# Kernel optimization log

Hardware: AMD Instinct MI355X
Metric: run time of the kernel (lower is better)

## Reference

```python
import jax, jax.numpy as jnp
import numpy as np

E = 1024
H = 16
HD = E // H  # 64
R = 8
ALPHA = 32
SCALING = ALPHA / R  # LoRA scaling = 4.0


def _lora_linear(x, W, b, A, B):
    # x: [..., in], W: [out, in], A: [r, in], B: [out, r]
    base = jnp.einsum('...i,oi->...o', x, W) + b
    lora = jnp.einsum('...r,or->...o', jnp.einsum('...i,ri->...r', x, A), B) * SCALING
    return base + lora


def setup_inputs() -> dict:
    key = jax.random.key(0)
    ks = jax.random.split(key, 20)
    L, N = 2048, 2
    d = {}
    d['query'] = jax.random.normal(ks[0], (L, N, E), dtype=jnp.float32)
    d['key_padding_mask'] = jax.random.randint(ks[1], (N, L), 0, 2) > 0
    i = 2
    for p in ('q', 'k', 'v', 'o'):
        d['W' + p] = jax.random.normal(ks[i], (E, E), dtype=jnp.float32) * (E ** -0.5); i += 1
        d['b' + p] = jax.random.normal(ks[i], (E,), dtype=jnp.float32) * 0.01; i += 1
        d['A' + p] = jax.random.normal(ks[i], (R, E), dtype=jnp.float32) * (E ** -0.5); i += 1
        d['B' + p] = jax.random.normal(ks[i], (E, R), dtype=jnp.float32) * 0.01; i += 1
    return d


def reference(query, key_padding_mask, Wq, bq, Aq, Bq, Wk, bk, Ak, Bk,
              Wv, bv, Av, Bv, Wo, bo, Ao, Bo):
    L, N, _ = query.shape
    q = _lora_linear(query, Wq, bq, Aq, Bq)  # [L, N, E]
    k = _lora_linear(query, Wk, bk, Ak, Bk)
    v = _lora_linear(query, Wv, bv, Av, Bv)

    def split_heads(x):  # [L, N, E] -> [N, H, L, HD]
        return x.transpose(1, 0, 2).reshape(N, L, H, HD).transpose(0, 2, 1, 3)

    scale = HD ** -0.5
    qh = split_heads(q) * scale
    kh = split_heads(k)
    vh = split_heads(v)

    logits = jnp.einsum('nhqd,nhkd->nhqk', qh, kh)  # [N, H, L, L]
    dt = logits.dtype
    pad = key_padding_mask[:, None, None, :]  # [N, 1, 1, Lk]
    logits = jnp.where(pad, jnp.finfo(dt).min, logits)
    logits = logits - jnp.max(logits, axis=-1, keepdims=True)
    w = jax.nn.softmax(logits, axis=-1)
    # zero out padded keys then renormalize (faithful to the module)
    w = jnp.where(pad, jnp.zeros((), dt), w)
    denom = jnp.maximum(jnp.sum(w, axis=-1, keepdims=True), jnp.finfo(dt).tiny)
    w = w / denom

    out = jnp.einsum('nhqk,nhkd->nhqd', w, vh)  # [N, H, L, HD]
    out = out.transpose(0, 2, 1, 3).reshape(N, L, E).transpose(1, 0, 2)  # [L, N, E]
    attn_output = _lora_linear(out, Wo, bo, Ao, Bo)

    # average_attn_weights=True path: mean over heads, then permute(1,0,2)
    attn_weights_out = jnp.mean(w, axis=1).transpose(1, 0, 2)  # [Lq, N, Lk]
    return attn_output, attn_weights_out
```

## Files before the change

### kernel.cpp

```cpp
#include <hip/hip_runtime.h>
#include <stdint.h>


typedef __attribute__((ext_vector_type(8))) short short8;
typedef __attribute__((ext_vector_type(4))) float f32x4;

#define LORA_SCALING 4.0f
#define FTINY 1.1754943508222875e-38f

static __device__ __forceinline__ unsigned short f2bf(float f){
  unsigned u = __float_as_uint(f);
  u += 0x7fffu + ((u >> 16) & 1u);
  return (unsigned short)(u >> 16);
}
static __device__ __forceinline__ float bflo(unsigned u){ return __uint_as_float(u << 16); }
static __device__ __forceinline__ float bfhi(unsigned u){ return __uint_as_float(u & 0xffff0000u); }
static __device__ __forceinline__ unsigned pk2(float lo, float hi){
  return (unsigned)f2bf(lo) | ((unsigned)f2bf(hi) << 16);
}
static __device__ __forceinline__ unsigned cvtpk(float lo, float hi){
  unsigned r;
  asm("v_cvt_pk_bf16_f32 %0, %1, %2" : "=v"(r) : "v"(lo), "v"(hi));
  return r;
}
static __device__ __forceinline__ void gload16(const void* g, void* l){
  __builtin_amdgcn_global_load_lds(
      (const __attribute__((address_space(1))) unsigned int*)g,
      (__attribute__((address_space(3))) unsigned int*)l, 16, 0, 0);
}

union S8U { short8 v; uint2 u[2]; };

__global__ __launch_bounds__(256) void pack_bf16(const float* __restrict__ src,
                                                 unsigned short* __restrict__ dst)
{
  const size_t i = (size_t)blockIdx.x * 256 + threadIdx.x;
  const float4 f0 = ((const float4*)src)[i*2];
  const float4 f1 = ((const float4*)src)[i*2 + 1];
  ((uint4*)dst)[i] = make_uint4(pk2(f0.x,f0.y), pk2(f0.z,f0.w),
                                pk2(f1.x,f1.y), pk2(f1.z,f1.w));
}

__global__ __launch_bounds__(256) void xa_kernel(const unsigned short* __restrict__ X,
                                                 const float* __restrict__ A,
                                                 float* __restrict__ xa)
{
  __shared__ float red[4][8];
  const int t = blockIdx.x, tid = threadIdx.x;
  const int lane = tid & 63, wid = tid >> 6;

  const uint2 xr = *(const uint2*)(X + (size_t)t*1024 + tid*4);
  const float x0 = bflo(xr.x), x1 = bfhi(xr.x), x2 = bflo(xr.y), x3 = bfhi(xr.y);

  float acc[8];
#pragma unroll
  for (int r = 0; r < 8; ++r) {
    const float4 ar = *(const float4*)(A + (size_t)r*1024 + tid*4);
    acc[r] = x0*ar.x + x1*ar.y + x2*ar.z + x3*ar.w;
  }
#pragma unroll
  for (int r = 0; r < 8; ++r) {
    float v = acc[r];
#pragma unroll
    for (int off = 32; off > 0; off >>= 1) v += __shfl_xor(v, off, 64);
    if (lane == 0) red[wid][r] = v;
  }
  __syncthreads();
  if (tid < 8) xa[(size_t)t*8 + tid] = red[0][tid] + red[1][tid] + red[2][tid] + red[3][tid];
}

__global__ __launch_bounds__(256) void gemm_bf16(
    const unsigned short* __restrict__ Abf,
    const unsigned short* __restrict__ W0bf, const unsigned short* __restrict__ W1bf,
    const unsigned short* __restrict__ W2bf,
    const float* __restrict__ B0, const float* __restrict__ B1, const float* __restrict__ B2,
    const float* __restrict__ xa0, const float* __restrict__ xa1, const float* __restrict__ xa2,
    const float* __restrict__ L0, const float* __restrict__ L1, const float* __restrict__ L2,
    void* __restrict__ C0, void* __restrict__ C1, void* __restrict__ C2,
    int fp32out, float scale0)
{
  const int z = blockIdx.z;
  const unsigned short* W = (z==0)?W0bf:((z==1)?W1bf:W2bf);
  const float* Bb = (z==0)?B0:((z==1)?B1:B2);
  const float* xa = (z==0)?xa0:((z==1)?xa1:xa2);
  const float* Lb = (z==0)?L0:((z==1)?L1:L2);
  void*        C  = (z==0)?C0:((z==1)?C1:C2);
  const bool vtw = (z == 2);
  const float sc = (z == 0) ? scale0 : 1.0f;

  __shared__ alignas(16) unsigned short As[128*32];
  __shared__ alignas(16) unsigned short Bs[128*32];

  const int tid = threadIdx.x;
  const int lane = tid & 63, wid = tid >> 6;
  const int quad = lane >> 4, lm = lane & 15;
  const int t0 = blockIdx.x * 128, n0 = blockIdx.y * 128;
  const int wm = (wid & 1) * 64, wn = (wid >> 1) * 64;

  const int c0 = tid, c1 = tid + 256;
  const int r0c = c0 >> 2, e0c = (c0 & 3) * 8;
  const int r1c = c1 >> 2, e1c = (c1 & 3) * 8;

  f32x4 acc[4][4];
#pragma unroll
  for (int i = 0; i < 4; ++i)
#pragma unroll
    for (int j = 0; j < 4; ++j) acc[i][j] = 0.f;

  for (int kt = 0; kt < 32; ++kt) {
    const int k0 = kt * 32;
    __syncthreads();
    gload16(Abf + (size_t)(t0 + r0c)*1024 + k0 + e0c, &As[c0*8]);
    gload16(Abf + (size_t)(t0 + r1c)*1024 + k0 + e1c, &As[c1*8]);
    gload16(W   + (size_t)(n0 + r0c)*1024 + k0 + e0c, &Bs[c0*8]);
    gload16(W   + (size_t)(n0 + r1c)*1024 + k0 + e1c, &Bs[c1*8]);
    __syncthreads();
    short8 a[4], b[4];
#pragma unroll
    for (int i = 0; i < 4; ++i) a[i] = *(const short8*)&As[(wm + i*16 + lm)*32 + quad*8];
#pragma unroll
    for (int j = 0; j < 4; ++j) b[j] = *(const short8*)&Bs[(wn + j*16 + lm)*32 + quad*8];
#pragma unroll
    for (int i = 0; i < 4; ++i)
#pragma unroll
      for (int j = 0; j < 4; ++j)
        acc[i][j] = __builtin_amdgcn_mfma_f32_16x16x32_bf16(a[i], b[j], acc[i][j], 0, 0, 0);
  }

#pragma unroll
  for (int j = 0; j < 4; ++j) {
    const int col = n0 + wn + j*16 + lm;
    const float bias = Bb[col];
    const float4 u0 = ((const float4*)(Lb + (size_t)col*8))[0];
    const float4 u1 = ((const float4*)(Lb + (size_t)col*8))[1];
#pragma unroll
    for (int i = 0; i < 4; ++i) {
#pragma unroll
      for (int r = 0; r < 4; ++r) {
        const int row = t0 + wm + i*16 + quad*4 + r;
        const float* xr = xa + (size_t)row*8;
        const float lora = xr[0]*u0.x + xr[1]*u0.y + xr[2]*u0.z + xr[3]*u0.w
                         + xr[4]*u1.x + xr[5]*u1.y + xr[6]*u1.z + xr[7]*u1.w;
        const float val = (acc[i][j][r] + bias + LORA_SCALING*lora) * sc;
        if (fp32out) {
          ((float*)C)[(size_t)row*1024 + col] = val;
        } else if (vtw) {
          ((unsigned short*)C)[((size_t)(row & 1) * 1024 + col) * 2048 + (row >> 1)] = f2bf(val);
        } else {
          ((unsigned short*)C)[(size_t)row*1024 + col] = f2bf(val);
        }
      }
    }
  }
}

__global__ __launch_bounds__(256) void attn_pv(
    const unsigned short* __restrict__ qb, const unsigned short* __restrict__ kb,
    const unsigned short* __restrict__ vt, const int* __restrict__ mask,
    unsigned short* __restrict__ ctx, float* __restrict__ msl)
{
  __shared__ alignas(16) unsigned short Es[128*132];
  __shared__ unsigned char mlds[2048];
  __shared__ float lred[2][128];

  const int tid = threadIdx.x, lane = tid & 63, wid = tid >> 6;
  const int quad = lane >> 4, lm = lane & 15;
  const int q0 = blockIdx.x * 128, n = blockIdx.y, h = blockIdx.z;
  const int wq = wid >> 1, wj = wid & 1;

  {
    const int4 m0 = *(const int4*)(mask + n*2048 + tid*8);
    const int4 m1 = *(const int4*)(mask + n*2048 + tid*8 + 4);
    mlds[tid*8+0] = (m0.x != 0); mlds[tid*8+1] = (m0.y != 0);
    mlds[tid*8+2] = (m0.z != 0); mlds[tid*8+3] = (m0.w != 0);
    mlds[tid*8+4] = (m1.x != 0); mlds[tid*8+5] = (m1.y != 0);
    mlds[tid*8+6] = (m1.z != 0); mlds[tid*8+7] = (m1.w != 0);
  }

  short8 bq[4][2];
#pragma unroll
  for (int q_t = 0; q_t < 4; ++q_t) {
    const unsigned short* qg = qb + ((size_t)(q0 + wq*64 + q_t*16 + lm)*2 + n)*1024 + h*64 + quad*8;
    bq[q_t][0] = *(const short8*)qg;
    bq[q_t][1] = *(const short8*)(qg + 32);
  }

  float lsum[4] = {0.f, 0.f, 0.f, 0.f};
  f32x4 oacc[2][4];
#pragma unroll
  for (int i2 = 0; i2 < 2; ++i2)
#pragma unroll
    for (int dt = 0; dt < 4; ++dt) oacc[i2][dt] = 0.f;

  for (int jt = 0; jt < 16; ++jt) {
    const int j0 = jt * 128;
    __syncthreads();

    f32x4 sacc[4][4];
#pragma unroll
    for (int a = 0; a < 4; ++a)
#pragma unroll
      for (int b = 0; b < 4; ++b) sacc[a][b] = 0.f;
#pragma unroll
    for (int kt = 0; kt < 2; ++kt) {
      short8 ak[4];
#pragma unroll
      for (int j_t = 0; j_t < 4; ++j_t)
        ak[j_t] = *(const short8*)(kb + ((size_t)(j0 + wj*64 + j_t*16 + lm)*2 + n)*1024 + h*64 + kt*32 + quad*8);
#pragma unroll
      for (int j_t = 0; j_t < 4; ++j_t)
#pragma unroll
        for (int q_t = 0; q_t < 4; ++q_t)
          sacc[j_t][q_t] = __builtin_amdgcn_mfma_f32_16x16x32_bf16(ak[j_t], bq[q_t][kt], sacc[j_t][q_t], 0, 0, 0);
    }
#pragma unroll
    for (int j_t = 0; j_t < 4; ++j_t) {
      const int jrow = wj*64 + j_t*16 + quad*4;
      const uchar4 mk = *(const uchar4*)&mlds[j0 + jrow];
#pragma unroll
      for (int q_t = 0; q_t < 4; ++q_t) {
        const float e0 = mk.x ? 0.f : __expf(sacc[j_t][q_t][0]);
        const float e1 = mk.y ? 0.f : __expf(sacc[j_t][q_t][1]);
        const float e2 = mk.z ? 0.f : __expf(sacc[j_t][q_t][2]);
        const float e3 = mk.w ? 0.f : __expf(sacc[j_t][q_t][3]);
        lsum[q_t] += (e0 + e1) + (e2 + e3);
        const int qcol = wq*64 + q_t*16 + lm;
        *(uint2*)&Es[qcol*132 + jrow] = make_uint2(cvtpk(e0, e1), cvtpk(e2, e3));
      }
    }
    __syncthreads();
#pragma unroll
    for (int kk = 0; kk < 4; ++kk) {
      S8U ae0, ae1;
      const int r0 = wid*32 + lm, r1 = r0 + 16;
      ae0.u[0] = *(const uint2*)&Es[r0*132 + kk*32 + quad*8];
      ae0.u[1] = *(const uint2*)&Es[r0*132 + kk*32 + quad*8 + 4];
      ae1.u[0] = *(const uint2*)&Es[r1*132 + kk*32 + quad*8];
      ae1.u[1] = *(const uint2*)&Es[r1*132 + kk*32 + quad*8 + 4];
      const unsigned short* vbase = vt + (size_t)((n*16 + h)*64)*2048 + j0 + kk*32 + quad*8;
#pragma unroll
      for (int dt = 0; dt < 4; ++dt) {
        const short8 bv = *(const short8*)(vbase + (size_t)(dt*16 + lm)*2048);
        oacc[0][dt] = __builtin_amdgcn_mfma_f32_16x16x32_bf16(ae0.v, bv, oacc[0][dt], 0, 0, 0);
        oacc[1][dt] = __builtin_amdgcn_mfma_f32_16x16x32_bf16(ae1.v, bv, oacc[1][dt], 0, 0, 0);
      }
    }
  }

#pragma unroll
  for (int q_t = 0; q_t < 4; ++q_t) {
    float v = lsum[q_t];
    v += __shfl_xor(v, 16, 64);
    v += __shfl_xor(v, 32, 64);
    if (quad == 0) lred[wj][wq*64 + q_t*16 + lm] = v;
  }
  __syncthreads();
  if (tid < 128) {
    const float l = lred[0][tid] + lred[1][tid];
    const float rinv = 1.0f / fmaxf(l, FTINY);
    lred[0][tid] = rinv;
    msl[(size_t)(h*2 + n)*2048 + q0 + tid] = rinv;
  }
  __syncthreads();
#pragma unroll
  for (int i2 = 0; i2 < 2; ++i2) {
    const int rb = wid*32 + i2*16 + quad*4;
    const float4 rv4 = *(const float4*)&lred[0][rb];
    const float rva[4] = {rv4.x, rv4.y, rv4.z, rv4.w};
#pragma unroll
    for (int dt = 0; dt < 4; ++dt) {
#pragma unroll
      for (int r = 0; r < 4; ++r) {
        ctx[((size_t)(q0 + rb + r)*2 + n)*1024 + h*64 + dt*16 + lm] =
            f2bf(oacc[i2][dt][r] * rva[r]);
      }
    }
  }
}

__global__ __launch_bounds__(256) void wmean2(
    const unsigned short* __restrict__ qb, const unsigned short* __restrict__ kb,
    const int* __restrict__ mask, const float* __restrict__ msl,
    float* __restrict__ wout)
{
  const int tid = threadIdx.x, lane = tid & 63, wid = tid >> 6;
  const int quad = lane >> 4, lm = lane & 15;
  const int q0 = blockIdx.x * 128, j0 = blockIdx.y * 128, n = blockIdx.z;
  const int wq = wid >> 1, wj = wid & 1;

  unsigned fm = 0;
#pragma unroll
  for (int j_t = 0; j_t < 4; ++j_t)
    fm |= (mask[n*2048 + j0 + wj*64 + j_t*16 + lm] != 0 ? 1u : 0u) << j_t;

  f32x4 wacc[4][4];
#pragma unroll
  for (int i = 0; i < 4; ++i)
#pragma unroll
    for (int j = 0; j < 4; ++j) wacc[i][j] = 0.f;

  for (int h = 0; h < 16; ++h) {
    short8 aq[4][2];
#pragma unroll
    for (int i = 0; i < 4; ++i) {
      const unsigned short* qg = qb + ((size_t)(q0 + wq*64 + i*16 + lm)*2 + n)*1024 + h*64 + quad*8;
      aq[i][0] = *(const short8*)qg;
      aq[i][1] = *(const short8*)(qg + 32);
    }
    float4 rv[4];
#pragma unroll
    for (int i = 0; i < 4; ++i)
      rv[i] = *(const float4*)&msl[(size_t)(h*2 + n)*2048 + q0 + wq*64 + i*16 + quad*4];
#pragma unroll
    for (int jh2 = 0; jh2 < 2; ++jh2) {
      short8 bk[2][2];
#pragma unroll
      for (int jtl = 0; jtl < 2; ++jtl) {
        const unsigned short* kg = kb + ((size_t)(j0 + wj*64 + (jh2*2 + jtl)*16 + lm)*2 + n)*1024 + h*64 + quad*8;
        bk[jtl][0] = *(const short8*)kg;
        bk[jtl][1] = *(const short8*)(kg + 32);
      }
      f32x4 sacc[4][2];
#pragma unroll
      for (int i = 0; i < 4; ++i)
#pragma unroll
        for (int jtl = 0; jtl < 2; ++jtl) sacc[i][jtl] = 0.f;
#pragma unroll
      for (int kt = 0; kt < 2; ++kt)
#pragma unroll
        for (int i = 0; i < 4; ++i)
#pragma unroll
          for (int jtl = 0; jtl < 2; ++jtl)
            sacc[i][jtl] = __builtin_amdgcn_mfma_f32_16x16x32_bf16(aq[i][kt], bk[jtl][kt], sacc[i][jtl], 0, 0, 0);
#pragma unroll
      for (int i = 0; i < 4; ++i) {
        const float rva[4] = {rv[i].x, rv[i].y, rv[i].z, rv[i].w};
#pragma unroll
        for (int jtl = 0; jtl < 2; ++jtl) {
          const int j_t = jh2*2 + jtl;
          const bool mskd = (fm >> j_t) & 1u;
#pragma unroll
          for (int r = 0; r < 4; ++r) {
            const float e = mskd ? 0.f : __expf(sacc[i][jtl][r]) * rva[r];
            wacc[i][j_t][r] += e;
          }
        }
      }
    }
  }
#pragma unroll
  for (int i = 0; i < 4; ++i)
#pragma unroll
    for (int j_t = 0; j_t < 4; ++j_t)
#pragma unroll
      for (int r = 0; r < 4; ++r) {
        const int row = q0 + wq*64 + i*16 + quad*4 + r;
        const int col = j0 + wj*64 + j_t*16 + lm;
        wout[((size_t)row*2 + n)*2048 + col] = wacc[i][j_t][r] * 0.0625f;
      }
}

__global__ __launch_bounds__(256) void ctx_copy(const uint4* __restrict__ src,
                                                uint4* __restrict__ dst)
{
  const size_t i = (size_t)blockIdx.x * 256 + threadIdx.x;
  dst[i] = src[i];
}

extern "C" void kernel_launch(void* const* d_in, const int* in_sizes, int n_in,
                              void* d_out, int out_size, void* d_ws, size_t ws_size,
                              hipStream_t stream) {
  const float* x    = (const float*)d_in[0];
  const int*   mask = (const int*)d_in[1];
  const float* Wq = (const float*)d_in[2];  const float* bq = (const float*)d_in[3];
  const float* Aq = (const float*)d_in[4];  const float* Bq = (const float*)d_in[5];
  const float* Wk = (const float*)d_in[6];  const float* bk = (const float*)d_in[7];
  const float* Ak = (const float*)d_in[8];  const float* Bk = (const float*)d_in[9];
  const float* Wv = (const float*)d_in[10]; const float* bv = (const float*)d_in[11];
  const float* Av = (const float*)d_in[12]; const float* Bv = (const float*)d_in[13];
  const float* Wo = (const float*)d_in[14]; const float* bo = (const float*)d_in[15];
  const float* Ao = (const float*)d_in[16]; const float* Bo = (const float*)d_in[17];

  float* outF = (float*)d_out;
  float* woutF = outF + 4194304;

  unsigned short* kbuf = (unsigned short*)d_ws;
  unsigned short* vtb  = kbuf + 4194304;
  unsigned short* qbuf = vtb  + 4194304;

  float* xaq = woutF;
  float* xak = xaq + 32768;
  float* xav = xak + 32768;

  unsigned short* Xbf  = (unsigned short*)outF;
  unsigned short* Wqbf = (unsigned short*)(outF + 2097152);
  unsigned short* Wkbf = (unsigned short*)(outF + 2621440);
  unsigned short* Wvbf = (unsigned short*)(outF + 3145728);
  unsigned short* ctx16 = (unsigned short*)outF;
  float* msl = outF + 2359296;

  float* xao = (float*)vtb;
  unsigned short* Wobf = vtb + 524288;

  pack_bf16<<<dim3(2048), dim3(256), 0, stream>>>(x, Xbf);
  pack_bf16<<<dim3(512),  dim3(256), 0, stream>>>(Wq, Wqbf);
  pack_bf16<<<dim3(512),  dim3(256), 0, stream>>>(Wk, Wkbf);
  pack_bf16<<<dim3(512),  dim3(256), 0, stream>>>(Wv, Wvbf);

  xa_kernel<<<dim3(4096), dim3(256), 0, stream>>>(Xbf, Aq, xaq);
  xa_kernel<<<dim3(4096), dim3(256), 0, stream>>>(Xbf, Ak, xak);
  xa_kernel<<<dim3(4096), dim3(256), 0, stream>>>(Xbf, Av, xav);

  gemm_bf16<<<dim3(32, 8, 3), dim3(256), 0, stream>>>(
      Xbf, Wqbf, Wkbf, Wvbf, bq, bk, bv, xaq, xak, xav, Bq, Bk, Bv,
      qbuf, kbuf, vtb, 0, 0.125f);

  attn_pv<<<dim3(16, 2, 16), dim3(256), 0, stream>>>(qbuf, kbuf, vtb, mask, ctx16, msl);

  pack_bf16<<<dim3(512), dim3(256), 0, stream>>>(Wo, Wobf);

  wmean2<<<dim3(16, 16, 2), dim3(256), 0, stream>>>(qbuf, kbuf, mask, msl, woutF);

  ctx_copy<<<dim3(2048), dim3(256), 0, stream>>>((const uint4*)ctx16, (uint4*)kbuf);

  xa_kernel<<<dim3(4096), dim3(256), 0, stream>>>(kbuf, Ao, xao);

  gemm_bf16<<<dim3(32, 8, 1), dim3(256), 0, stream>>>(
      kbuf, Wobf, Wobf, Wobf, bo, bo, bo, xao, xao, xao, Bo, Bo, Bo,
      outF, outF, outF, 1, 1.0f);
}
```

Baseline: 472.5 us.

## Software-pipeline QK^T/exp of next key tile with PV of current tile

Double-buffers the exponentiated score tile in shared memory so that the QK^T MFMA, exp and store for key tile jt+1 are computed after the PV MFMAs for tile jt, with K loads issued early. This removes one barrier per iteration and lets global K/V loads overlap MFMA work. It also merges the three weight bf16 pack launches into a single launch to cut launch overhead. In exchange it doubles the score LDS buffer (about 67KB), which may lower occupancy, and raises register pressure from the prefetched K fragments.

```diff
diff --git a/kernel.cpp b/kernel.cpp
--- a/kernel.cpp
+++ b/kernel.cpp
@@ -34,6 +34,20 @@
 __global__ __launch_bounds__(256) void pack_bf16(const float* __restrict__ src,
                                                  unsigned short* __restrict__ dst)
 {
+  const size_t i = (size_t)blockIdx.x * 256 + threadIdx.x;
+  const float4 f0 = ((const float4*)src)[i*2];
+  const float4 f1 = ((const float4*)src)[i*2 + 1];
+  ((uint4*)dst)[i] = make_uint4(pk2(f0.x,f0.y), pk2(f0.z,f0.w),
+                                pk2(f1.x,f1.y), pk2(f1.z,f1.w));
+}
+__global__ __launch_bounds__(256) void pack3_bf16(
+    const float* __restrict__ s0, const float* __restrict__ s1, const float* __restrict__ s2,
+    unsigned short* __restrict__ d0, unsigned short* __restrict__ d1,
+    unsigned short* __restrict__ d2)
+{
+  const int z = blockIdx.y;
+  const float* src = (z==0)?s0:((z==1)?s1:s2);
+  unsigned short* dst = (z==0)?d0:((z==1)?d1:d2);
   const size_t i = (size_t)blockIdx.x * 256 + threadIdx.x;
   const float4 f0 = ((const float4*)src)[i*2];
   const float4 f1 = ((const float4*)src)[i*2 + 1];
@@ -159,7 +173,7 @@
     const unsigned short* __restrict__ vt, const int* __restrict__ mask,
     unsigned short* __restrict__ ctx, float* __restrict__ msl)
 {
-  __shared__ alignas(16) unsigned short Es[128*132];
+  __shared__ alignas(16) unsigned short Es[2][128*132];
   __shared__ unsigned char mlds[2048];
   __shared__ float lred[2][128];
 
@@ -192,57 +206,106 @@
 #pragma unroll
     for (int dt = 0; dt < 4; ++dt) oacc[i2][dt] = 0.f;
 
+  __syncthreads();
+
+#pragma unroll
+  for (int jp = 0; jp < 2; ++jp) {
+    f32x4 sacc[2][4];
+#pragma unroll
+    for (int a = 0; a < 2; ++a)
+#pragma unroll
+      for (int b = 0; b < 4; ++b) sacc[a][b] = 0.f;
+#pragma unroll
+    for (int kt = 0; kt < 2; ++kt) {
+      short8 ak[2];
+#pragma unroll
+      for (int jl = 0; jl < 2; ++jl)
+        ak[jl] = *(const short8*)(kb + ((size_t)(wj*64 + (jp*2+jl)*16 + lm)*2 + n)*1024 + h*64 + kt*32 + quad*8);
+#pragma unroll
+      for (int jl = 0; jl < 2; ++jl)
+#pragma unroll
+        for (int q_t = 0; q_t < 4; ++q_t)
+          sacc[jl][q_t] = __builtin_amdgcn_mfma_f32_16x16x32_bf16(ak[jl], bq[q_t][kt], sacc[jl][q_t], 0, 0, 0);
+    }
+#pragma unroll
+    for (int jl = 0; jl < 2; ++jl) {
+      const int jrow = wj*64 + (jp*2+jl)*16 + quad*4;
+      const uchar4 mk = *(const uchar4*)&mlds[jrow];
+#pragma unroll
+      for (int q_t = 0; q_t < 4; ++q_t) {
+        const float e0 = mk.x ? 0.f : __expf(sacc[jl][q_t][0]);
+        const float e1 = mk.y ? 0.f : __expf(sacc[jl][q_t][1]);
+        const float e2 = mk.z ? 0.f : __expf(sacc[jl][q_t][2]);
+        const float e3 = mk.w ? 0.f : __expf(sacc[jl][q_t][3]);
+        lsum[q_t] += (e0 + e1) + (e2 + e3);
+        const int qcol = wq*64 + q_t*16 + lm;
+        *(uint2*)&Es[0][qcol*132 + jrow] = make_uint2(cvtpk(e0, e1), cvtpk(e2, e3));
+      }
+    }
+  }
+
   for (int jt = 0; jt < 16; ++jt) {
+    const int cur = jt & 1;
     const int j0 = jt * 128;
     __syncthreads();
 
-    f32x4 sacc[4][4];
-#pragma unroll
-    for (int a = 0; a < 4; ++a)
-#pragma unroll
-      for (int b = 0; b < 4; ++b) sacc[a][b] = 0.f;
-#pragma unroll
-    for (int kt = 0; kt < 2; ++kt) {
-      short8 ak[4];
-#pragma unroll
-      for (int j_t = 0; j_t < 4; ++j_t)
-        ak[j_t] = *(const short8*)(kb + ((size_t)(j0 + wj*64 + j_t*16 + lm)*2 + n)*1024 + h*64 + kt*32 + quad*8);
-#pragma unroll
-      for (int j_t = 0; j_t < 4; ++j_t)
-#pragma unroll
-        for (int q_t = 0; q_t < 4; ++q_t)
-          sacc[j_t][q_t] = __builtin_amdgcn_mfma_f32_16x16x32_bf16(ak[j_t], bq[q_t][kt], sacc[j_t][q_t], 0, 0, 0);
-    }
-#pragma unroll
-    for (int j_t = 0; j_t < 4; ++j_t) {
-      const int jrow = wj*64 + j_t*16 + quad*4;
-      const uchar4 mk = *(const uchar4*)&mlds[j0 + jrow];
-#pragma unroll
-      for (int q_t = 0; q_t < 4; ++q_t) {
-        const float e0 = mk.x ? 0.f : __expf(sacc[j_t][q_t][0]);
-        const float e1 = mk.y ? 0.f : __expf(sacc[j_t][q_t][1]);
-        const float e2 = mk.z ? 0.f : __expf(sacc[j_t][q_t][2]);
-        const float e3 = mk.w ? 0.f : __expf(sacc[j_t][q_t][3]);
-        lsum[q_t] += (e0 + e1) + (e2 + e3);
-        const int qcol = wq*64 + q_t*16 + lm;
-        *(uint2*)&Es[qcol*132 + jrow] = make_uint2(cvtpk(e0, e1), cvtpk(e2, e3));
-      }
-    }
-    __syncthreads();
+    short8 akn[2][4];
+    if (jt < 15) {
+      const int j0n = j0 + 128;
+#pragma unroll
+      for (int kt = 0; kt < 2; ++kt)
+#pragma unroll
+        for (int j_t = 0; j_t < 4; ++j_t)
+          akn[kt][j_t] = *(const short8*)(kb + ((size_t)(j0n + wj*64 + j_t*16 + lm)*2 + n)*1024 + h*64 + kt*32 + quad*8);
+    }
+
 #pragma unroll
     for (int kk = 0; kk < 4; ++kk) {
       S8U ae0, ae1;
       const int r0 = wid*32 + lm, r1 = r0 + 16;
-      ae0.u[0] = *(const uint2*)&Es[r0*132 + kk*32 + quad*8];
-      ae0.u[1] = *(const uint2*)&Es[r0*132 + kk*32 + quad*8 + 4];
-      ae1.u[0] = *(const uint2*)&Es[r1*132 + kk*32 + quad*8];
-      ae1.u[1] = *(const uint2*)&Es[r1*132 + kk*32 + quad*8 + 4];
+      ae0.u[0] = *(const uint2*)&Es[cur][r0*132 + kk*32 + quad*8];
+      ae0.u[1] = *(const uint2*)&Es[cur][r0*132 + kk*32 + quad*8 + 4];
+      ae1.u[0] = *(const uint2*)&Es[cur][r1*132 + kk*32 + quad*8];
+      ae1.u[1] = *(const uint2*)&Es[cur][r1*132 + kk*32 + quad*8 + 4];
       const unsigned short* vbase = vt + (size_t)((n*16 + h)*64)*2048 + j0 + kk*32 + quad*8;
 #pragma unroll
       for (int dt = 0; dt < 4; ++dt) {
         const short8 bv = *(const short8*)(vbase + (size_t)(dt*16 + lm)*2048);
         oacc[0][dt] = __builtin_amdgcn_mfma_f32_16x16x32_bf16(ae0.v, bv, oacc[0][dt], 0, 0, 0);
         oacc[1][dt] = __builtin_amdgcn_mfma_f32_16x16x32_bf16(ae1.v, bv, oacc[1][dt], 0, 0, 0);
+      }
+    }
+
+    if (jt < 15) {
+#pragma unroll
+      for (int jp = 0; jp < 2; ++jp) {
+        f32x4 sacc[2][4];
+#pragma unroll
+        for (int a = 0; a < 2; ++a)
+#pragma unroll
+          for (int b = 0; b < 4; ++b) sacc[a][b] = 0.f;
+#pragma unroll
+        for (int kt = 0; kt < 2; ++kt)
+#pragma unroll
+          for (int jl = 0; jl < 2; ++jl)
+#pragma unroll
+            for (int q_t = 0; q_t < 4; ++q_t)
+              sacc[jl][q_t] = __builtin_amdgcn_mfma_f32_16x16x32_bf16(akn[kt][jp*2+jl], bq[q_t][kt], sacc[jl][q_t], 0, 0, 0);
+#pragma unroll
+        for (int jl = 0; jl < 2; ++jl) {
+          const int jrow = wj*64 + (jp*2+jl)*16 + quad*4;
+          const uchar4 mk = *(const uchar4*)&mlds[j0 + 128 + jrow];
+#pragma unroll
+          for (int q_t = 0; q_t < 4; ++q_t) {
+            const float e0 = mk.x ? 0.f : __expf(sacc[jl][q_t][0]);
+            const float e1 = mk.y ? 0.f : __expf(sacc[jl][q_t][1]);
+            const float e2 = mk.z ? 0.f : __expf(sacc[jl][q_t][2]);
+            const float e3 = mk.w ? 0.f : __expf(sacc[jl][q_t][3]);
+            lsum[q_t] += (e0 + e1) + (e2 + e3);
+            const int qcol = wq*64 + q_t*16 + lm;
+            *(uint2*)&Es[cur^1][qcol*132 + jrow] = make_uint2(cvtpk(e0, e1), cvtpk(e2, e3));
+          }
+        }
       }
     }
   }
@@ -403,9 +466,7 @@
   unsigned short* Wobf = vtb + 524288;
 
   pack_bf16<<<dim3(2048), dim3(256), 0, stream>>>(x, Xbf);
-  pack_bf16<<<dim3(512),  dim3(256), 0, stream>>>(Wq, Wqbf);
-  pack_bf16<<<dim3(512),  dim3(256), 0, stream>>>(Wk, Wkbf);
-  pack_bf16<<<dim3(512),  dim3(256), 0, stream>>>(Wv, Wvbf);
+  pack3_bf16<<<dim3(512, 3), dim3(256), 0, stream>>>(Wq, Wk, Wv, Wqbf, Wkbf, Wvbf);
 
   xa_kernel<<<dim3(4096), dim3(256), 0, stream>>>(Xbf, Aq, xaq);
   xa_kernel<<<dim3(4096), dim3(256), 0, stream>>>(Xbf, Ak, xak);
```

Result: no change. 474.2 us (+0.4%).

## Fold log2e into Q scale, use exp2 with additive mask bias, merge launches

Applied to the files above, without the earlier changes.

Q is now scaled by log2(e)/8, so both attention kernels can call the raw v_exp_f32 (exp2) directly instead of __expf. The key padding mask becomes an additive -3e38 bias preloaded as the MFMA accumulator init, which removes the per-element select. In the weight-mean kernel the per-row reciprocal and the 1/16 head factor are folded into a log2 offset added through the accumulator init, and masking moves to the final store. The three W packs and three xa launches are each merged into one launch over a grid z-dimension. The risk is that the huge negative bias passing through the MFMA accumulate and exp2 has to underflow cleanly to zero.

```diff
diff --git a/kernel.cpp b/kernel.cpp
--- a/kernel.cpp
+++ b/kernel.cpp
@@ -7,6 +7,7 @@
 
 #define LORA_SCALING 4.0f
 #define FTINY 1.1754943508222875e-38f
+#define QSCALE 0.18033688011112042f
 
 static __device__ __forceinline__ unsigned short f2bf(float f){
   unsigned u = __float_as_uint(f);
@@ -22,6 +23,19 @@
   unsigned r;
   asm("v_cvt_pk_bf16_f32 %0, %1, %2" : "=v"(r) : "v"(lo), "v"(hi));
   return r;
+}
+static __device__ __forceinline__ float vexp2(float x){
+  float r;
+  asm("v_exp_f32 %0, %1" : "=v"(r) : "v"(x));
+  return r;
+}
+static __device__ __forceinline__ float vlog2(float x){
+  float r;
+  asm("v_log_f32 %0, %1" : "=v"(r) : "v"(x));
+  return r;
+}
+static __device__ __forceinline__ f32x4 f4v(float4 t){
+  f32x4 v; v[0]=t.x; v[1]=t.y; v[2]=t.z; v[3]=t.w; return v;
 }
 static __device__ __forceinline__ void gload16(const void* g, void* l){
   __builtin_amdgcn_global_load_lds(
@@ -39,6 +53,53 @@
   const float4 f1 = ((const float4*)src)[i*2 + 1];
   ((uint4*)dst)[i] = make_uint4(pk2(f0.x,f0.y), pk2(f0.z,f0.w),
                                 pk2(f1.x,f1.y), pk2(f1.z,f1.w));
+}
+__global__ __launch_bounds__(256) void pack3_bf16(
+    const float* __restrict__ s0, const float* __restrict__ s1, const float* __restrict__ s2,
+    unsigned short* __restrict__ d0, unsigned short* __restrict__ d1,
+    unsigned short* __restrict__ d2)
+{
+  const int z = blockIdx.y;
+  const float* src = (z==0)?s0:((z==1)?s1:s2);
+  unsigned short* dst = (z==0)?d0:((z==1)?d1:d2);
+  const size_t i = (size_t)blockIdx.x * 256 + threadIdx.x;
+  const float4 f0 = ((const float4*)src)[i*2];
+  const float4 f1 = ((const float4*)src)[i*2 + 1];
+  ((uint4*)dst)[i] = make_uint4(pk2(f0.x,f0.y), pk2(f0.z,f0.w),
+                                pk2(f1.x,f1.y), pk2(f1.z,f1.w));
+}
+
+__global__ __launch_bounds__(256) void xa3_kernel(
+    const unsigned short* __restrict__ X,
+    const float* __restrict__ A0, const float* __restrict__ A1,
+    const float* __restrict__ A2,
+    float* __restrict__ x0p, float* __restrict__ x1p, float* __restrict__ x2p)
+{
+  __shared__ float red[4][8];
+  const int z = blockIdx.y;
+  const float* A = (z==0)?A0:((z==1)?A1:A2);
+  float* xa = (z==0)?x0p:((z==1)?x1p:x2p);
+  const int t = blockIdx.x, tid = threadIdx.x;
+  const int lane = tid & 63, wid = tid >> 6;
+
+  const uint2 xr = *(const uint2*)(X + (size_t)t*1024 + tid*4);
+  const float x0 = bflo(xr.x), x1 = bfhi(xr.x), x2 = bflo(xr.y), x3 = bfhi(xr.y);
+
+  float acc[8];
+#pragma unroll
+  for (int r = 0; r < 8; ++r) {
+    const float4 ar = *(const float4*)(A + (size_t)r*1024 + tid*4);
+    acc[r] = x0*ar.x + x1*ar.y + x2*ar.z + x3*ar.w;
+  }
+#pragma unroll
+  for (int r = 0; r < 8; ++r) {
+    float v = acc[r];
+#pragma unroll
+    for (int off = 32; off > 0; off >>= 1) v += __shfl_xor(v, off, 64);
+    if (lane == 0) red[wid][r] = v;
+  }
+  __syncthreads();
+  if (tid < 8) xa[(size_t)t*8 + tid] = red[0][tid] + red[1][tid] + red[2][tid] + red[3][tid];
 }
 
 __global__ __launch_bounds__(256) void xa_kernel(const unsigned short* __restrict__ X,
@@ -160,7 +221,7 @@
     unsigned short* __restrict__ ctx, float* __restrict__ msl)
 {
   __shared__ alignas(16) unsigned short Es[128*132];
-  __shared__ unsigned char mlds[2048];
+  __shared__ float mbias[2048];
   __shared__ float lred[2][128];
 
   const int tid = threadIdx.x, lane = tid & 63, wid = tid >> 6;
@@ -171,10 +232,14 @@
   {
     const int4 m0 = *(const int4*)(mask + n*2048 + tid*8);
     const int4 m1 = *(const int4*)(mask + n*2048 + tid*8 + 4);
-    mlds[tid*8+0] = (m0.x != 0); mlds[tid*8+1] = (m0.y != 0);
-    mlds[tid*8+2] = (m0.z != 0); mlds[tid*8+3] = (m0.w != 0);
-    mlds[tid*8+4] = (m1.x != 0); mlds[tid*8+5] = (m1.y != 0);
-    mlds[tid*8+6] = (m1.z != 0); mlds[tid*8+7] = (m1.w != 0);
+    mbias[tid*8+0] = m0.x ? -3.0e38f : 0.f;
+    mbias[tid*8+1] = m0.y ? -3.0e38f : 0.f;
+    mbias[tid*8+2] = m0.z ? -3.0e38f : 0.f;
+    mbias[tid*8+3] = m0.w ? -3.0e38f : 0.f;
+    mbias[tid*8+4] = m1.x ? -3.0e38f : 0.f;
+    mbias[tid*8+5] = m1.y ? -3.0e38f : 0.f;
+    mbias[tid*8+6] = m1.z ? -3.0e38f : 0.f;
+    mbias[tid*8+7] = m1.w ? -3.0e38f : 0.f;
   }
 
   short8 bq[4][2];
@@ -198,31 +263,36 @@
 
     f32x4 sacc[4][4];
 #pragma unroll
-    for (int a = 0; a < 4; ++a)
-#pragma unroll
-      for (int b = 0; b < 4; ++b) sacc[a][b] = 0.f;
-#pragma unroll
     for (int kt = 0; kt < 2; ++kt) {
       short8 ak[4];
 #pragma unroll
       for (int j_t = 0; j_t < 4; ++j_t)
         ak[j_t] = *(const short8*)(kb + ((size_t)(j0 + wj*64 + j_t*16 + lm)*2 + n)*1024 + h*64 + kt*32 + quad*8);
-#pragma unroll
-      for (int j_t = 0; j_t < 4; ++j_t)
-#pragma unroll
-        for (int q_t = 0; q_t < 4; ++q_t)
-          sacc[j_t][q_t] = __builtin_amdgcn_mfma_f32_16x16x32_bf16(ak[j_t], bq[q_t][kt], sacc[j_t][q_t], 0, 0, 0);
+      if (kt == 0) {
+#pragma unroll
+        for (int j_t = 0; j_t < 4; ++j_t) {
+          const f32x4 bini = f4v(*(const float4*)&mbias[j0 + wj*64 + j_t*16 + quad*4]);
+#pragma unroll
+          for (int q_t = 0; q_t < 4; ++q_t)
+            sacc[j_t][q_t] = __builtin_amdgcn_mfma_f32_16x16x32_bf16(ak[j_t], bq[q_t][0], bini, 0, 0, 0);
+        }
+      } else {
+#pragma unroll
+        for (int j_t = 0; j_t < 4; ++j_t)
+#pragma unroll
+          for (int q_t = 0; q_t < 4; ++q_t)
+            sacc[j_t][q_t] = __builtin_amdgcn_mfma_f32_16x16x32_bf16(ak[j_t], bq[q_t][1], sacc[j_t][q_t], 0, 0, 0);
+      }
     }
 #pragma unroll
     for (int j_t = 0; j_t < 4; ++j_t) {
       const int jrow = wj*64 + j_t*16 + quad*4;
-      const uchar4 mk = *(const uchar4*)&mlds[j0 + jrow];
 #pragma unroll
       for (int q_t = 0; q_t < 4; ++q_t) {
-        const float e0 = mk.x ? 0.f : __expf(sacc[j_t][q_t][0]);
-        const float e1 = mk.y ? 0.f : __expf(sacc[j_t][q_t][1]);
-        const float e2 = mk.z ? 0.f : __expf(sacc[j_t][q_t][2]);
-        const float e3 = mk.w ? 0.f : __expf(sacc[j_t][q_t][3]);
+        const float e0 = vexp2(sacc[j_t][q_t][0]);
+        const float e1 = vexp2(sacc[j_t][q_t][1]);
+        const float e2 = vexp2(sacc[j_t][q_t][2]);
+        const float e3 = vexp2(sacc[j_t][q_t][3]);
         lsum[q_t] += (e0 + e1) + (e2 + e3);
         const int qcol = wq*64 + q_t*16 + lm;
         *(uint2*)&Es[qcol*132 + jrow] = make_uint2(cvtpk(e0, e1), cvtpk(e2, e3));
@@ -256,10 +326,9 @@
   }
   __syncthreads();
   if (tid < 128) {
-    const float l = lred[0][tid] + lred[1][tid];
-    const float rinv = 1.0f / fmaxf(l, FTINY);
-    lred[0][tid] = rinv;
-    msl[(size_t)(h*2 + n)*2048 + q0 + tid] = rinv;
+    const float l = fmaxf(lred[0][tid] + lred[1][tid], FTINY);
+    lred[0][tid] = 1.0f / l;
+    msl[(size_t)(h*2 + n)*2048 + q0 + tid] = -vlog2(l) - 4.0f;
   }
   __syncthreads();
 #pragma unroll
@@ -307,10 +376,10 @@
       aq[i][0] = *(const short8*)qg;
       aq[i][1] = *(const short8*)(qg + 32);
     }
-    float4 rv[4];
+    f32x4 lr[4];
 #pragma unroll
     for (int i = 0; i < 4; ++i)
-      rv[i] = *(const float4*)&msl[(size_t)(h*2 + n)*2048 + q0 + wq*64 + i*16 + quad*4];
+      lr[i] = f4v(*(const float4*)&msl[(size_t)(h*2 + n)*2048 + q0 + wq*64 + i*16 + quad*4]);
 #pragma unroll
     for (int jh2 = 0; jh2 < 2; ++jh2) {
       short8 bk[2][2];
@@ -324,40 +393,36 @@
 #pragma unroll
       for (int i = 0; i < 4; ++i)
 #pragma unroll
-        for (int jtl = 0; jtl < 2; ++jtl) sacc[i][jtl] = 0.f;
-#pragma unroll
-      for (int kt = 0; kt < 2; ++kt)
-#pragma unroll
-        for (int i = 0; i < 4; ++i)
-#pragma unroll
-          for (int jtl = 0; jtl < 2; ++jtl)
-            sacc[i][jtl] = __builtin_amdgcn_mfma_f32_16x16x32_bf16(aq[i][kt], bk[jtl][kt], sacc[i][jtl], 0, 0, 0);
-#pragma unroll
-      for (int i = 0; i < 4; ++i) {
-        const float rva[4] = {rv[i].x, rv[i].y, rv[i].z, rv[i].w};
+        for (int jtl = 0; jtl < 2; ++jtl)
+          sacc[i][jtl] = __builtin_amdgcn_mfma_f32_16x16x32_bf16(aq[i][0], bk[jtl][0], lr[i], 0, 0, 0);
+#pragma unroll
+      for (int i = 0; i < 4; ++i)
+#pragma unroll
+        for (int jtl = 0; jtl < 2; ++jtl)
+          sacc[i][jtl] = __builtin_amdgcn_mfma_f32_16x16x32_bf16(aq[i][1], bk[jtl][1], sacc[i][jtl], 0, 0, 0);
+#pragma unroll
+      for (int i = 0; i < 4; ++i)
 #pragma unroll
         for (int jtl = 0; jtl < 2; ++jtl) {
           const int j_t = jh2*2 + jtl;
-          const bool mskd = (fm >> j_t) & 1u;
-#pragma unroll
-          for (int r = 0; r < 4; ++r) {
-            const float e = mskd ? 0.f : __expf(sacc[i][jtl][r]) * rva[r];
-            wacc[i][j_t][r] += e;
-          }
+#pragma unroll
+          for (int r = 0; r < 4; ++r)
+            wacc[i][j_t][r] += vexp2(sacc[i][jtl][r]);
         }
-      }
     }
   }
 #pragma unroll
   for (int i = 0; i < 4; ++i)
 #pragma unroll
-    for (int j_t = 0; j_t < 4; ++j_t)
+    for (int j_t = 0; j_t < 4; ++j_t) {
+      const bool mskd = (fm >> j_t) & 1u;
 #pragma unroll
       for (int r = 0; r < 4; ++r) {
         const int row = q0 + wq*64 + i*16 + quad*4 + r;
         const int col = j0 + wj*64 + j_t*16 + lm;
-        wout[((size_t)row*2 + n)*2048 + col] = wacc[i][j_t][r] * 0.0625f;
-      }
+        wout[((size_t)row*2 + n)*2048 + col] = mskd ? 0.f : wacc[i][j_t][r];
+      }
+    }
 }
 
 __global__ __launch_bounds__(256) void ctx_copy(const uint4* __restrict__ src,
@@ -403,17 +468,13 @@
   unsigned short* Wobf = vtb + 524288;
 
   pack_bf16<<<dim3(2048), dim3(256), 0, stream>>>(x, Xbf);
-  pack_bf16<<<dim3(512),  dim3(256), 0, stream>>>(Wq, Wqbf);
-  pack_bf16<<<dim3(512),  dim3(256), 0, stream>>>(Wk, Wkbf);
-  pack_bf16<<<dim3(512),  dim3(256), 0, stream>>>(Wv, Wvbf);
-
-  xa_kernel<<<dim3(4096), dim3(256), 0, stream>>>(Xbf, Aq, xaq);
-  xa_kernel<<<dim3(4096), dim3(256), 0, stream>>>(Xbf, Ak, xak);
-  xa_kernel<<<dim3(4096), dim3(256), 0, stream>>>(Xbf, Av, xav);
+  pack3_bf16<<<dim3(512, 3), dim3(256), 0, stream>>>(Wq, Wk, Wv, Wqbf, Wkbf, Wvbf);
+
+  xa3_kernel<<<dim3(4096, 3), dim3(256), 0, stream>>>(Xbf, Aq, Ak, Av, xaq, xak, xav);
 
   gemm_bf16<<<dim3(32, 8, 3), dim3(256), 0, stream>>>(
       Xbf, Wqbf, Wkbf, Wvbf, bq, bk, bv, xaq, xak, xav, Bq, Bk, Bv,
-      qbuf, kbuf, vtb, 0, 0.125f);
+      qbuf, kbuf, vtb, 0, QSCALE);
 
   attn_pv<<<dim3(16, 2, 16), dim3(256), 0, stream>>>(qbuf, kbuf, vtb, mask, ctx16, msl);
 
```

Result: faster. 462.0 us (-2.2%).
